# Kernel tuning notes

Hardware: AMD Instinct MI355X
Metric: run time of the kernel (lower is better)

The kernel has to match this reference:

```python
import jax, jax.numpy as jnp
import numpy as np


def setup_inputs() -> dict:
    key = jax.random.key(0)
    k1, k2 = jax.random.split(key)
    B, N, S, C = 8, 65536, 4, 8
    psi = jax.random.normal(k1, (B, N, S), dtype=jnp.float32)
    # nn.Parameter(torch.randn(d_coord, d_spinor, d_spinor) / sqrt(d_spinor))
    gamma = jax.random.normal(k2, (C, S, S), dtype=jnp.float32) / jnp.sqrt(jnp.float32(S))
    return {"psi": psi, "gamma": gamma}


def reference(psi, gamma):
    # G[mu,nu] = gamma[mu] @ gamma[nu]  -> [C, C, S, S]
    G = jnp.einsum('mij,njk->mnik', gamma, gamma)
    Gt = jnp.swapaxes(G, 0, 1)                 # G[nu,mu]
    A = 0.5 * (G - Gt)                         # 0.5 * commutator  (K1 generator)
    Ssym = 0.5 * (G + Gt)                      # 0.5 * anticommutator (K2 generator)

    # K0: sigma = psi_bar psi (psi_bar == psi here)
    K0 = jnp.einsum('bni,bni->bn', psi, psi)   # [B, N]

    # Precompute small outer product per token, then contract once per output.
    outer = jnp.einsum('bni,bnj->bnij', psi, psi)   # [B, N, S, S] (small S=4)
    K1 = jnp.einsum('bnij,mnuv->bnmn'.replace('nu', 'x'), outer, A) if False else \
         jnp.einsum('bnij,cdij->bncd', outer, A)    # [B, N, C, C] antisymmetric
    K2 = jnp.einsum('bnij,cdij->bncd', outer, Ssym) # [B, N, C, C] symmetric
    return (K0, K1, K2)
```

## Files before the change

### kernel.cpp

```cpp
#include <hip/hip_runtime.h>


#define TPB 128
#define LDS_STRIDE 68

__device__ __forceinline__ float dot4(float4 a, float4 b) {
    return a.x * b.x + a.y * b.y + a.z * b.z + a.w * b.w;
}

__global__ __launch_bounds__(TPB) void spinor_bilinears_kernel(
    const float* __restrict__ psi,
    const float* __restrict__ gamma,
    float* __restrict__ out,
    long long n_tokens) {
    __shared__ float ldsT[TPB * LDS_STRIDE];

    const int tid = threadIdx.x;
    const long long t_glob = (long long)blockIdx.x * TPB + tid;

    float* K0 = out;
    float* K1 = out + n_tokens;
    float* K2 = out + n_tokens + n_tokens * 64;

    const float4 p = ((const float4*)psi)[t_glob];

    K0[t_glob] = dot4(p, p);

    float4 u[8], v[8];
    const float4* g4 = (const float4*)gamma;
#pragma unroll
    for (int c = 0; c < 8; ++c) {
        const float4 g0 = g4[c * 4 + 0];
        const float4 g1 = g4[c * 4 + 1];
        const float4 g2 = g4[c * 4 + 2];
        const float4 g3 = g4[c * 4 + 3];
        float4 uc;
        uc.x = p.x * g0.x + p.y * g1.x + p.z * g2.x + p.w * g3.x;
        uc.y = p.x * g0.y + p.y * g1.y + p.z * g2.y + p.w * g3.y;
        uc.z = p.x * g0.z + p.y * g1.z + p.z * g2.z + p.w * g3.z;
        uc.w = p.x * g0.w + p.y * g1.w + p.z * g2.w + p.w * g3.w;
        u[c] = uc;
        float4 vc;
        vc.x = dot4(g0, p);
        vc.y = dot4(g1, p);
        vc.z = dot4(g2, p);
        vc.w = dot4(g3, p);
        v[c] = vc;
    }

    float* row = &ldsT[tid * LDS_STRIDE];
#pragma unroll
    for (int c = 0; c < 8; ++c) {
        float4 t0, t1;
        t0.x = dot4(u[c], v[0]);
        t0.y = dot4(u[c], v[1]);
        t0.z = dot4(u[c], v[2]);
        t0.w = dot4(u[c], v[3]);
        t1.x = dot4(u[c], v[4]);
        t1.y = dot4(u[c], v[5]);
        t1.z = dot4(u[c], v[6]);
        t1.w = dot4(u[c], v[7]);
        ((float4*)(row + c * 8))[0] = t0;
        ((float4*)(row + c * 8))[1] = t1;
    }

    __syncthreads();

    const long long blk_base = (long long)blockIdx.x * (TPB * 64);
    float4* K1v = (float4*)(K1 + blk_base);
    float4* K2v = (float4*)(K2 + blk_base);

    const int cd0 = (tid & 15) * 4;
    const int c = cd0 >> 3;
    const int d0 = cd0 & 7;

#pragma unroll
    for (int it = 0; it < 16; ++it) {
        const int t = it * 8 + (tid >> 4);
        const float* trow = &ldsT[t * LDS_STRIDE];
        const float4 tcd = *(const float4*)(trow + cd0);
        const float td0 = trow[(d0 + 0) * 8 + c];
        const float td1 = trow[(d0 + 1) * 8 + c];
        const float td2 = trow[(d0 + 2) * 8 + c];
        const float td3 = trow[(d0 + 3) * 8 + c];

        float4 k1v, k2v;
        k1v.x = 0.5f * (tcd.x - td0);  k2v.x = 0.5f * (tcd.x + td0);
        k1v.y = 0.5f * (tcd.y - td1);  k2v.y = 0.5f * (tcd.y + td1);
        k1v.z = 0.5f * (tcd.z - td2);  k2v.z = 0.5f * (tcd.z + td2);
        k1v.w = 0.5f * (tcd.w - td3);  k2v.w = 0.5f * (tcd.w + td3);

        K1v[it * 128 + tid] = k1v;
        K2v[it * 128 + tid] = k2v;
    }
}

extern "C" void kernel_launch(void* const* d_in, const int* in_sizes, int n_in,
                              void* d_out, int out_size, void* d_ws, size_t ws_size,
                              hipStream_t stream) {
    const float* psi = (const float*)d_in[0];
    const float* gamma = (const float*)d_in[1];
    float* out = (float*)d_out;

    const long long n_tokens = (long long)in_sizes[0] / 4;
    const int blocks = (int)(n_tokens / TPB);

    spinor_bilinears_kernel<<<blocks, TPB, 0, stream>>>(psi, gamma, out, n_tokens);
}
```

Baseline: 268.4 us.

## Keep per-token 8x8 product in registers and stage output through per-wave LDS

The 8x8 per-token matrix T now stays in registers, and each thread computes the antisymmetric and symmetric parts directly, so the block-wide LDS transpose and __syncthreads are gone. Results go in four chunks through small per-wave LDS buffers (stride 17, wave barriers only) and are written out as coalesced float4 stores. The block grows to 256 threads, the 0.5 factor is folded into u, and indexing moves to 32-bit. In exchange, register pressure rises because 64 floats are held per thread, and the hand-coded waitcnt immediate could be wrong if the encoding differs.

```diff
diff --git a/kernel.cpp b/kernel.cpp
--- a/kernel.cpp
+++ b/kernel.cpp
@@ -1,97 +1,83 @@
 #include <hip/hip_runtime.h>
 
 
-#define TPB 128
-#define LDS_STRIDE 68
+#define TPB 256
+#define STG 17
 
 __device__ __forceinline__ float dot4(float4 a, float4 b) {
     return a.x * b.x + a.y * b.y + a.z * b.z + a.w * b.w;
 }
 
-__global__ __launch_bounds__(TPB) void spinor_bilinears_kernel(
+__global__ __launch_bounds__(TPB, 4) void spinor_bilinears_kernel(
     const float* __restrict__ psi,
     const float* __restrict__ gamma,
     float* __restrict__ out,
-    long long n_tokens) {
-    __shared__ float ldsT[TPB * LDS_STRIDE];
+    int n_tokens) {
+    __shared__ float stgA[4][64 * STG];
+    __shared__ float stgB[4][64 * STG];
 
-    const int tid = threadIdx.x;
-    const long long t_glob = (long long)blockIdx.x * TPB + tid;
+    const int tid  = threadIdx.x;
+    const int wave = tid >> 6;
+    const int lane = tid & 63;
+    const int g0   = blockIdx.x * TPB + (wave << 6);
+    const int g    = g0 + lane;
 
-    float* K0 = out;
-    float* K1 = out + n_tokens;
-    float* K2 = out + n_tokens + n_tokens * 64;
+    float*  K0  = out;
+    float4* K1v = (float4*)(out + n_tokens);
+    float4* K2v = (float4*)(out + n_tokens + (size_t)n_tokens * 64);
 
-    const float4 p = ((const float4*)psi)[t_glob];
-
-    K0[t_glob] = dot4(p, p);
+    const float4 p = ((const float4*)psi)[g];
+    K0[g] = dot4(p, p);
+    const float4 ph = make_float4(0.5f * p.x, 0.5f * p.y, 0.5f * p.z, 0.5f * p.w);
 
     float4 u[8], v[8];
     const float4* g4 = (const float4*)gamma;
 #pragma unroll
     for (int c = 0; c < 8; ++c) {
-        const float4 g0 = g4[c * 4 + 0];
-        const float4 g1 = g4[c * 4 + 1];
-        const float4 g2 = g4[c * 4 + 2];
-        const float4 g3 = g4[c * 4 + 3];
-        float4 uc;
-        uc.x = p.x * g0.x + p.y * g1.x + p.z * g2.x + p.w * g3.x;
-        uc.y = p.x * g0.y + p.y * g1.y + p.z * g2.y + p.w * g3.y;
-        uc.z = p.x * g0.z + p.y * g1.z + p.z * g2.z + p.w * g3.z;
-        uc.w = p.x * g0.w + p.y * g1.w + p.z * g2.w + p.w * g3.w;
-        u[c] = uc;
-        float4 vc;
-        vc.x = dot4(g0, p);
-        vc.y = dot4(g1, p);
-        vc.z = dot4(g2, p);
-        vc.w = dot4(g3, p);
-        v[c] = vc;
+        const float4 r0 = g4[c * 4 + 0];
+        const float4 r1 = g4[c * 4 + 1];
+        const float4 r2 = g4[c * 4 + 2];
+        const float4 r3 = g4[c * 4 + 3];
+        u[c] = make_float4(ph.x * r0.x + ph.y * r1.x + ph.z * r2.x + ph.w * r3.x,
+                           ph.x * r0.y + ph.y * r1.y + ph.z * r2.y + ph.w * r3.y,
+                           ph.x * r0.z + ph.y * r1.z + ph.z * r2.z + ph.w * r3.z,
+                           ph.x * r0.w + ph.y * r1.w + ph.z * r2.w + ph.w * r3.w);
+        v[c] = make_float4(dot4(r0, p), dot4(r1, p), dot4(r2, p), dot4(r3, p));
     }
 
-    float* row = &ldsT[tid * LDS_STRIDE];
+    float T[8][8];
 #pragma unroll
-    for (int c = 0; c < 8; ++c) {
-        float4 t0, t1;
-        t0.x = dot4(u[c], v[0]);
-        t0.y = dot4(u[c], v[1]);
-        t0.z = dot4(u[c], v[2]);
-        t0.w = dot4(u[c], v[3]);
-        t1.x = dot4(u[c], v[4]);
-        t1.y = dot4(u[c], v[5]);
-        t1.z = dot4(u[c], v[6]);
-        t1.w = dot4(u[c], v[7]);
-        ((float4*)(row + c * 8))[0] = t0;
-        ((float4*)(row + c * 8))[1] = t1;
-    }
+    for (int c = 0; c < 8; ++c)
+#pragma unroll
+        for (int d = 0; d < 8; ++d)
+            T[c][d] = dot4(u[c], v[d]);
 
-    __syncthreads();
-
-    const long long blk_base = (long long)blockIdx.x * (TPB * 64);
-    float4* K1v = (float4*)(K1 + blk_base);
-    float4* K2v = (float4*)(K2 + blk_base);
-
-    const int cd0 = (tid & 15) * 4;
-    const int c = cd0 >> 3;
-    const int d0 = cd0 & 7;
+    float* A = &stgA[wave][0];
+    float* B = &stgB[wave][0];
 
 #pragma unroll
-    for (int it = 0; it < 16; ++it) {
-        const int t = it * 8 + (tid >> 4);
-        const float* trow = &ldsT[t * LDS_STRIDE];
-        const float4 tcd = *(const float4*)(trow + cd0);
-        const float td0 = trow[(d0 + 0) * 8 + c];
-        const float td1 = trow[(d0 + 1) * 8 + c];
-        const float td2 = trow[(d0 + 2) * 8 + c];
-        const float td3 = trow[(d0 + 3) * 8 + c];
+    for (int k = 0; k < 4; ++k) {
+#pragma unroll
+        for (int f = 0; f < 16; ++f) {
+            const int c = 2 * k + (f >> 3);
+            const int d = f & 7;
+            A[lane * STG + f] = T[c][d] - T[d][c];
+            B[lane * STG + f] = T[c][d] + T[d][c];
+        }
+        __builtin_amdgcn_s_waitcnt(0xC07F);
+        __builtin_amdgcn_wave_barrier();
 
-        float4 k1v, k2v;
-        k1v.x = 0.5f * (tcd.x - td0);  k2v.x = 0.5f * (tcd.x + td0);
-        k1v.y = 0.5f * (tcd.y - td1);  k2v.y = 0.5f * (tcd.y + td1);
-        k1v.z = 0.5f * (tcd.z - td2);  k2v.z = 0.5f * (tcd.z + td2);
-        k1v.w = 0.5f * (tcd.w - td3);  k2v.w = 0.5f * (tcd.w + td3);
-
-        K1v[it * 128 + tid] = k1v;
-        K2v[it * 128 + tid] = k2v;
+#pragma unroll
+        for (int s = 0; s < 4; ++s) {
+            const int trow = (s << 4) + (lane >> 2);
+            const int rb   = trow * STG + (lane & 3) * 4;
+            const float4 av = make_float4(A[rb], A[rb + 1], A[rb + 2], A[rb + 3]);
+            const float4 bv = make_float4(B[rb], B[rb + 1], B[rb + 2], B[rb + 3]);
+            const int f4i = ((g0 + trow) << 4) + (k << 2) + (lane & 3);
+            K1v[f4i] = av;
+            K2v[f4i] = bv;
+        }
+        __builtin_amdgcn_wave_barrier();
     }
 }
 
@@ -102,8 +88,8 @@
     const float* gamma = (const float*)d_in[1];
     float* out = (float*)d_out;
 
-    const long long n_tokens = (long long)in_sizes[0] / 4;
-    const int blocks = (int)(n_tokens / TPB);
+    const int n_tokens = in_sizes[0] / 4;
+    const int blocks = n_tokens / TPB;
 
     spinor_bilinears_kernel<<<blocks, TPB, 0, stream>>>(psi, gamma, out, n_tokens);
 }
```

Result: slower. 322.6 us (+20.2%).
